# Kernel optimization log

Hardware: AMD Instinct MI355X
Metric: run time of the kernel (lower is better)

## Reference

```python
import jax, jax.numpy as jnp
import numpy as np

B, S, D, H = 2, 4096, 768, 12
DEPTH = D // H


def setup_inputs() -> dict:
    key = jax.random.key(0)
    ks = jax.random.split(key, 6)
    return {
        "q": jax.random.normal(ks[0], (B, S, D), dtype=jnp.float32),
        "k": jax.random.normal(ks[1], (B, S, D), dtype=jnp.float32),
        "v": jax.random.normal(ks[2], (B, S, D), dtype=jnp.float32),
        "wq": jax.random.normal(ks[3], (D, D), dtype=jnp.float32),
        "wk": jax.random.normal(ks[4], (D, D), dtype=jnp.float32),
        "wv": jax.random.normal(ks[5], (D, D), dtype=jnp.float32),
    }


def _split_heads(x):
    # [B, S, D] -> [B, H, S, depth]
    b, s, _ = x.shape
    return x.reshape(b, s, H, DEPTH).transpose(0, 2, 1, 3)


def reference(q, k, v, wq, wk, wv):
    qh = _split_heads(q @ wq)  # [B,H,S,dh]
    kh = _split_heads(k @ wk)
    vh = _split_heads(v @ wv)
    scale = 1.0 / jnp.sqrt(jnp.asarray(DEPTH, dtype=qh.dtype))
    scores = jnp.einsum("bhqd,bhkd->bhqk", qh, kh) * scale  # [B,H,S,S]
    attn = jax.nn.softmax(scores, axis=-1)
    out = jnp.einsum("bhqk,bhkd->bhqd", attn, vh)  # [B,H,S,dh]
    return out.transpose(0, 2, 1, 3).reshape(q.shape[0], -1, D)
```

## Files before the change

### kernel.cpp

```cpp
#include <hip/hip_runtime.h>
#include <cstdint>

#define B_   2
#define S_   4096
#define D_   768
#define H_   12
#define DH_  64
#define BH_  (B_*H_)
#define M_   (B_*S_)

typedef _Float16 fp16;
typedef __attribute__((ext_vector_type(8))) _Float16 fp16x8;
typedef __attribute__((ext_vector_type(4))) _Float16 fp16x4;
typedef __attribute__((ext_vector_type(4))) float    f32x4;

#define MFMA16(a,b,c) __builtin_amdgcn_mfma_f32_16x16x32_f16((a),(b),(c),0,0,0)

__device__ __forceinline__ float exp2_hw(float x) {
  float r; asm("v_exp_f32 %0, %1" : "=v"(r) : "v"(x)); return r;
}
__device__ __forceinline__ uint32_t pkrtz(float a, float b) {
  uint32_t r; asm("v_cvt_pkrtz_f16_f32 %0, %1, %2" : "=v"(r) : "v"(a), "v"(b));
  return r;
}

__device__ __forceinline__ void gld_lds16(const void* g, void* l) {
  __builtin_amdgcn_global_load_lds(
      (const __attribute__((address_space(1))) unsigned int*)g,
      (__attribute__((address_space(3))) unsigned int*)l, 16, 0, 0);
}

__device__ __forceinline__ void stage64x128(const char* gbase, int pitch,
                                            char* lds, int tid) {
  const int lane = tid & 63, wv = tid >> 6;
#pragma unroll
  for (int j = 0; j < 2; ++j) {
    const int o   = (wv*2 + j)*1024 + lane*16;
    const int row = o >> 7;
    const int cb  = (o & 127) ^ ((row & 7) << 4);
    gld_lds16(gbase + (size_t)row*pitch + cb, lds + (wv*2 + j)*1024);
  }
}

__global__ __launch_bounds__(256) void prep_w(const float* __restrict__ wq,
                                              const float* __restrict__ wk,
                                              const float* __restrict__ wv,
                                              fp16* __restrict__ wt) {
  const int idx = blockIdx.x*256 + threadIdx.x;
  const int mat = idx / (768*768);
  const int e   = idx % (768*768);
  const int n   = e / 768, k = e % 768;
  const float* w = mat == 0 ? wq : (mat == 1 ? wk : wv);
  const float v = w[(size_t)k*768 + n];
  fp16* base = wt + (size_t)mat * (2*768*768);
  const fp16 hv = (fp16)v;
  base[e]            = hv;
  base[768*768 + e]  = (fp16)(v - (float)hv);
}

__global__ __launch_bounds__(256) void proj_gemm(
    const float* __restrict__ xq, const float* __restrict__ xk,
    const float* __restrict__ xv, const fp16* __restrict__ wt,
    fp16* __restrict__ qhi, fp16* __restrict__ qlo,
    fp16* __restrict__ khi, fp16* __restrict__ klo,
    fp16* __restrict__ vtp) {
  __shared__ __align__(16) char sm[16384];
  char* sWh = sm;
  char* sWl = sm + 8192;
  const int tid = threadIdx.x, lane = tid & 63, wv = tid >> 6;
  const int c = lane & 15, g = lane >> 4;
  const int r128 = c * 128;
  const int co0 = ((c & 7) ^ g) << 4;
  const int co1 = co0 ^ 64;
  const int mb  = blockIdx.x * 64;
  const int h   = blockIdx.y;
  const int nb  = h * 64;
  const int mat = blockIdx.z;
  const float* x = mat == 0 ? xq : (mat == 1 ? xk : xv);
  const fp16* wth = wt + (size_t)mat * (2*768*768);
  const fp16* wtl = wth + 768*768;

  f32x4 acc[4] = {};
  const int xrow = mb + wv*16 + c;

  for (int k0 = 0; k0 < 768; k0 += 64) {
    __syncthreads();
    stage64x128((const char*)(wth + (size_t)nb*768 + k0), 1536, sWh, tid);
    stage64x128((const char*)(wtl + (size_t)nb*768 + k0), 1536, sWl, tid);
    __syncthreads();

    fp16x8 ah[2], al[2];
#pragma unroll
    for (int ks = 0; ks < 2; ++ks) {
      const float* xp = x + (size_t)xrow*768 + k0 + ks*32 + g*8;
      const f32x4 x0 = *(const f32x4*)xp;
      const f32x4 x1 = *(const f32x4*)(xp + 4);
#pragma unroll
      for (int j = 0; j < 8; ++j) {
        const float v = j < 4 ? x0[j] : x1[j - 4];
        const fp16 hv = (fp16)v;
        ah[ks][j] = hv;
        al[ks][j] = (fp16)(v - (float)hv);
      }
    }
#pragma unroll
    for (int ks = 0; ks < 2; ++ks)
#pragma unroll
      for (int nt = 0; nt < 4; ++nt) {
        const char* wb  = sWh + r128 + nt*2048;
        const char* wlb = sWl + r128 + nt*2048;
        const int co = ks ? co1 : co0;
        const fp16x8 bh = *(const fp16x8*)(wb  + co);
        const fp16x8 bl = *(const fp16x8*)(wlb + co);
        acc[nt] = MFMA16(ah[ks], bh, acc[nt]);
        acc[nt] = MFMA16(ah[ks], bl, acc[nt]);
        acc[nt] = MFMA16(al[ks], bh, acc[nt]);
      }
  }

  if (mat < 2) {
    fp16* ph = mat ? khi : qhi;
    fp16* pl = mat ? klo : qlo;
#pragma unroll
    for (int nt = 0; nt < 4; ++nt)
#pragma unroll
      for (int r = 0; r < 4; ++r) {
        const int m = mb + wv*16 + g*4 + r;
        const int bb = m >> 12, s = m & (S_-1);
        const size_t idx = ((size_t)(bb*H_ + h)*S_ + s)*DH_ + nt*16 + c;
        const float v = acc[nt][r];
        const fp16 hv = (fp16)v;
        ph[idx] = hv;
        pl[idx] = (fp16)(v - (float)hv);
      }
  } else {
    __syncthreads();
    fp16* tile = (fp16*)sm;
#pragma unroll
    for (int nt = 0; nt < 4; ++nt) {
      const int dd = nt*16 + c, ml = wv*16 + g*4;
      const fp16x4 hv = {(fp16)acc[nt][0], (fp16)acc[nt][1],
                         (fp16)acc[nt][2], (fp16)acc[nt][3]};
      *(fp16x4*)(tile + dd*64 + ml) = hv;
    }
    __syncthreads();
    const int bb = mb >> 12, s0 = mb & (S_-1);
    const int dd = tid >> 2, ml0 = (tid & 3) * 16;
    const size_t obase = ((size_t)(bb*H_ + h)*DH_ + dd)*S_ + s0 + ml0;
#pragma unroll
    for (int u = 0; u < 2; ++u)
      *(fp16x8*)(vtp + obase + u*8) = *(const fp16x8*)(tile + dd*64 + ml0 + u*8);
  }
}

__global__ __launch_bounds__(256) void mha_flash(
    const fp16* __restrict__ qhi, const fp16* __restrict__ qlo,
    const fp16* __restrict__ khi, const fp16* __restrict__ klo,
    const fp16* __restrict__ vt, float* __restrict__ out) {
  __shared__ __align__(16) char sm[40960];
  char* sKh = sm;
  char* sKl = sm + 8192;
  char* sV  = sm + 16384;
  char* sP  = sm + 24576;

  const int tid = threadIdx.x, lane = tid & 63, wv = tid >> 6;
  const int c = lane & 15, g = lane >> 4;
  const int r128 = c * 128;
  const int co0 = ((c & 7) ^ g) << 4;
  const int co1 = co0 ^ 64;
  const int pg3 = (g & 1) << 3;
  const int pse = ((c & 7) ^ (g >> 1)) << 4;
  const int qb = blockIdx.x * 128;
  const int bh = blockIdx.y;
  const int b = bh / H_, h = bh % H_;

  const size_t qoff = ((size_t)bh*S_ + qb) * DH_;
  stage64x128((const char*)(qhi + qoff),          128, sm,         tid);
  stage64x128((const char*)(qhi + qoff + 64*DH_), 128, sm +  8192, tid);
  stage64x128((const char*)(qlo + qoff),          128, sm + 16384, tid);
  stage64x128((const char*)(qlo + qoff + 64*DH_), 128, sm + 24576, tid);
  __syncthreads();

  fp16x8 qfh[2][2], qfl[2][2];
  {
    const char* hb = sm + (wv >> 1)*8192;
    const char* lb = sm + 16384 + (wv >> 1)*8192;
#pragma unroll
    for (int qs = 0; qs < 2; ++qs) {
      const int rl = ((wv & 1)*32 + qs*16 + c) * 128;
      qfh[qs][0] = *(const fp16x8*)(hb + rl + co0);
      qfh[qs][1] = *(const fp16x8*)(hb + rl + co1);
      qfl[qs][0] = *(const fp16x8*)(lb + rl + co0);
      qfl[qs][1] = *(const fp16x8*)(lb + rl + co1);
    }
  }

  float m_run[2] = {-1e30f, -1e30f};
  float lrow[2][4] = {};
  f32x4 accO[2][4] = {};
  fp16x8 ones;
#pragma unroll
  for (int j = 0; j < 8; ++j) ones[j] = (fp16)1.0f;
  const float C2 = 0.125f * 1.4426950408889634f;

  for (int kt = 0; kt < S_/64; ++kt) {
    __syncthreads();
    const size_t koff = ((size_t)bh*S_ + kt*64) * DH_;
    stage64x128((const char*)(khi + koff), 128, sKh, tid);
    stage64x128((const char*)(klo + koff), 128, sKl, tid);
    stage64x128((const char*)(vt + (size_t)bh*DH_*S_ + kt*64), S_*2, sV, tid);
    __syncthreads();

    f32x4 accS[2][4] = {};
#pragma unroll
    for (int t = 0; t < 4; ++t) {
      const char* kb = sKh + r128 + t*2048;
      const char* lb = sKl + r128 + t*2048;
      const fp16x8 kh0 = *(const fp16x8*)(kb + co0);
      const fp16x8 kh1 = *(const fp16x8*)(kb + co1);
      const fp16x8 kl0 = *(const fp16x8*)(lb + co0);
      const fp16x8 kl1 = *(const fp16x8*)(lb + co1);
#pragma unroll
      for (int qs = 0; qs < 2; ++qs) {
        accS[qs][t] = MFMA16(kh0, qfh[qs][0], accS[qs][t]);
        accS[qs][t] = MFMA16(kh0, qfl[qs][0], accS[qs][t]);
        accS[qs][t] = MFMA16(kl0, qfh[qs][0], accS[qs][t]);
        accS[qs][t] = MFMA16(kh1, qfh[qs][1], accS[qs][t]);
        accS[qs][t] = MFMA16(kh1, qfl[qs][1], accS[qs][t]);
        accS[qs][t] = MFMA16(kl1, qfh[qs][1], accS[qs][t]);
      }
    }

    float mx0 = -1e30f, mx1 = -1e30f;
#pragma unroll
    for (int t = 0; t < 4; ++t) {
      mx0 = fmaxf(mx0, fmaxf(fmaxf(accS[0][t][0], accS[0][t][1]),
                             fmaxf(accS[0][t][2], accS[0][t][3])));
      mx1 = fmaxf(mx1, fmaxf(fmaxf(accS[1][t][0], accS[1][t][1]),
                             fmaxf(accS[1][t][2], accS[1][t][3])));
    }
    mx0 = fmaxf(mx0, __shfl_xor(mx0, 16));
    mx0 = fmaxf(mx0, __shfl_xor(mx0, 32));
    mx1 = fmaxf(mx1, __shfl_xor(mx1, 16));
    mx1 = fmaxf(mx1, __shfl_xor(mx1, 32));

    const bool rec = (mx0 > m_run[0]) || (mx1 > m_run[1]);
    if (__any(rec)) {
#pragma unroll
      for (int qs = 0; qs < 2; ++qs) {
        const float mxq = qs ? mx1 : mx0;
        const float m_new = fmaxf(m_run[qs], mxq);
        const float corr = exp2_hw(__builtin_fmaf(m_run[qs], C2, -m_new*C2));
        m_run[qs] = m_new;
        float crow[4];
#pragma unroll
        for (int r = 0; r < 4; ++r)
          crow[r] = __shfl(corr, (lane & 48) | (g*4 + r));
#pragma unroll
        for (int r = 0; r < 4; ++r) lrow[qs][r] *= crow[r];
#pragma unroll
        for (int d = 0; d < 4; ++d)
#pragma unroll
          for (int r = 0; r < 4; ++r) accO[qs][d][r] *= crow[r];
      }
    }

    char* pbase = sP + wv*4096 + r128;
#pragma unroll
    for (int qs = 0; qs < 2; ++qs) {
      const float negnm = -m_run[qs]*C2;
      char* pb = pbase + qs*2048;
#pragma unroll
      for (int t = 0; t < 4; ++t) {
        const float p0 = exp2_hw(__builtin_fmaf(accS[qs][t][0], C2, negnm));
        const float p1 = exp2_hw(__builtin_fmaf(accS[qs][t][1], C2, negnm));
        const float p2 = exp2_hw(__builtin_fmaf(accS[qs][t][2], C2, negnm));
        const float p3 = exp2_hw(__builtin_fmaf(accS[qs][t][3], C2, negnm));
        uint2 pw; pw.x = pkrtz(p0, p1); pw.y = pkrtz(p2, p3);
        *(uint2*)(pb + (pg3 | (pse ^ (t*32)))) = pw;
      }
    }

    const fp16x8 pA0 = *(const fp16x8*)(pbase + co0);
    const fp16x8 pA1 = *(const fp16x8*)(pbase + co1);
    const fp16x8 pB0 = *(const fp16x8*)(pbase + 2048 + co0);
    const fp16x8 pB1 = *(const fp16x8*)(pbase + 2048 + co1);
    f32x4 aL0 = {}, aL1 = {};
    aL0 = MFMA16(pA0, ones, aL0);
    aL0 = MFMA16(pA1, ones, aL0);
    aL1 = MFMA16(pB0, ones, aL1);
    aL1 = MFMA16(pB1, ones, aL1);
#pragma unroll
    for (int d = 0; d < 4; ++d) {
      const char* vb = sV + r128 + d*2048;
      const fp16x8 v0 = *(const fp16x8*)(vb + co0);
      const fp16x8 v1 = *(const fp16x8*)(vb + co1);
      accO[0][d] = MFMA16(pA0, v0, accO[0][d]);
      accO[0][d] = MFMA16(pA1, v1, accO[0][d]);
      accO[1][d] = MFMA16(pB0, v0, accO[1][d]);
      accO[1][d] = MFMA16(pB1, v1, accO[1][d]);
    }
#pragma unroll
    for (int r = 0; r < 4; ++r) {
      lrow[0][r] += aL0[r];
      lrow[1][r] += aL1[r];
    }
  }

#pragma unroll
  for (int qs = 0; qs < 2; ++qs) {
    float inv[4];
#pragma unroll
    for (int r = 0; r < 4; ++r) inv[r] = 1.f / lrow[qs][r];
    const int s0 = qb + wv*32 + qs*16 + g*4;
#pragma unroll
    for (int d = 0; d < 4; ++d)
#pragma unroll
      for (int r = 0; r < 4; ++r)
        out[((size_t)(b*S_ + s0 + r))*D_ + h*DH_ + d*16 + c] =
            accO[qs][d][r] * inv[r];
  }
}

extern "C" void kernel_launch(void* const* d_in, const int* in_sizes, int n_in,
                              void* d_out, int out_size, void* d_ws, size_t ws_size,
                              hipStream_t stream) {
  const float* xq = (const float*)d_in[0];
  const float* xk = (const float*)d_in[1];
  const float* xv = (const float*)d_in[2];
  const float* wq = (const float*)d_in[3];
  const float* wk = (const float*)d_in[4];
  const float* wv = (const float*)d_in[5];
  float* out = (float*)d_out;

  fp16* wt  = (fp16*)d_ws;
  fp16* qhi = wt + (size_t)6*768*768;
  const size_t PL = (size_t)BH_*S_*DH_;
  fp16* qlo = qhi + PL;
  fp16* khi = qlo + PL;
  fp16* klo = khi + PL;
  fp16* vtp = klo + PL;

  hipLaunchKernelGGL(prep_w, dim3(3*768*768/256), dim3(256), 0, stream,
                     wq, wk, wv, wt);
  hipLaunchKernelGGL(proj_gemm, dim3(M_/64, H_, 3), dim3(256), 0, stream,
                     xq, xk, xv, wt, qhi, qlo, khi, klo, vtp);
  hipLaunchKernelGGL(mha_flash, dim3(S_/128, BH_), dim3(256), 0, stream,
                     qhi, qlo, khi, klo, vtp, out);
}
```

Before: 514.5 us.

## Double-buffer K tiles, prefetch next K during PV, split P per half

The K hi/lo tiles are now double-buffered. The next tile's K is staged after the mid-iteration barrier, so its global-load latency overlaps the P·V MFMAs. V is staged at the top of each iteration, which removes one of the two leading barriers. The P scratch is halved by processing the two 16-row query halves one after another through the same buffer. s_setprio hints are placed around the MFMA blocks. LDS grows from 40KB to 48KB per block, which may reduce resident blocks per CU.

```diff
diff --git a/kernel.cpp b/kernel.cpp
--- a/kernel.cpp
+++ b/kernel.cpp
@@ -157,11 +157,13 @@
     const fp16* __restrict__ qhi, const fp16* __restrict__ qlo,
     const fp16* __restrict__ khi, const fp16* __restrict__ klo,
     const fp16* __restrict__ vt, float* __restrict__ out) {
-  __shared__ __align__(16) char sm[40960];
-  char* sKh = sm;
-  char* sKl = sm + 8192;
-  char* sV  = sm + 16384;
-  char* sP  = sm + 24576;
+  __shared__ __align__(16) char sm[49152];
+  char* sKh0 = sm;
+  char* sKl0 = sm + 8192;
+  char* sKh1 = sm + 16384;
+  char* sKl1 = sm + 24576;
+  char* sV   = sm + 32768;
+  char* sP   = sm + 40960;
 
   const int tid = threadIdx.x, lane = tid & 63, wv = tid >> 6;
   const int c = lane & 15, g = lane >> 4;
@@ -194,6 +196,13 @@
       qfl[qs][1] = *(const fp16x8*)(lb + rl + co1);
     }
   }
+  __syncthreads();
+
+  const size_t kbase = (size_t)bh * S_ * DH_;
+  const size_t vbase = (size_t)bh * DH_ * S_;
+  stage64x128((const char*)(khi + kbase), 128, sKh0, tid);
+  stage64x128((const char*)(klo + kbase), 128, sKl0, tid);
+  __syncthreads();
 
   float m_run[2] = {-1e30f, -1e30f};
   float lrow[2][4] = {};
@@ -204,18 +213,19 @@
   const float C2 = 0.125f * 1.4426950408889634f;
 
   for (int kt = 0; kt < S_/64; ++kt) {
-    __syncthreads();
-    const size_t koff = ((size_t)bh*S_ + kt*64) * DH_;
-    stage64x128((const char*)(khi + koff), 128, sKh, tid);
-    stage64x128((const char*)(klo + koff), 128, sKl, tid);
-    stage64x128((const char*)(vt + (size_t)bh*DH_*S_ + kt*64), S_*2, sV, tid);
-    __syncthreads();
+    char* sKhC = (kt & 1) ? sKh1 : sKh0;
+    char* sKlC = (kt & 1) ? sKl1 : sKl0;
+    char* sKhN = (kt & 1) ? sKh0 : sKh1;
+    char* sKlN = (kt & 1) ? sKl0 : sKl1;
+
+    stage64x128((const char*)(vt + vbase + kt*64), S_*2, sV, tid);
 
     f32x4 accS[2][4] = {};
+    __builtin_amdgcn_s_setprio(1);
 #pragma unroll
     for (int t = 0; t < 4; ++t) {
-      const char* kb = sKh + r128 + t*2048;
-      const char* lb = sKl + r128 + t*2048;
+      const char* kb = sKhC + r128 + t*2048;
+      const char* lb = sKlC + r128 + t*2048;
       const fp16x8 kh0 = *(const fp16x8*)(kb + co0);
       const fp16x8 kh1 = *(const fp16x8*)(kb + co1);
       const fp16x8 kl0 = *(const fp16x8*)(lb + co0);
@@ -230,6 +240,7 @@
         accS[qs][t] = MFMA16(kl1, qfh[qs][1], accS[qs][t]);
       }
     }
+    __builtin_amdgcn_s_setprio(0);
 
     float mx0 = -1e30f, mx1 = -1e30f;
 #pragma unroll
@@ -265,46 +276,76 @@
       }
     }
 
-    char* pbase = sP + wv*4096 + r128;
-#pragma unroll
-    for (int qs = 0; qs < 2; ++qs) {
-      const float negnm = -m_run[qs]*C2;
-      char* pb = pbase + qs*2048;
+    char* pbase = sP + wv*2048 + r128;
+    {
+      const float negnm = -m_run[0]*C2;
 #pragma unroll
       for (int t = 0; t < 4; ++t) {
-        const float p0 = exp2_hw(__builtin_fmaf(accS[qs][t][0], C2, negnm));
-        const float p1 = exp2_hw(__builtin_fmaf(accS[qs][t][1], C2, negnm));
-        const float p2 = exp2_hw(__builtin_fmaf(accS[qs][t][2], C2, negnm));
-        const float p3 = exp2_hw(__builtin_fmaf(accS[qs][t][3], C2, negnm));
+        const float p0 = exp2_hw(__builtin_fmaf(accS[0][t][0], C2, negnm));
+        const float p1 = exp2_hw(__builtin_fmaf(accS[0][t][1], C2, negnm));
+        const float p2 = exp2_hw(__builtin_fmaf(accS[0][t][2], C2, negnm));
+        const float p3 = exp2_hw(__builtin_fmaf(accS[0][t][3], C2, negnm));
         uint2 pw; pw.x = pkrtz(p0, p1); pw.y = pkrtz(p2, p3);
-        *(uint2*)(pb + (pg3 | (pse ^ (t*32)))) = pw;
-      }
-    }
-
-    const fp16x8 pA0 = *(const fp16x8*)(pbase + co0);
-    const fp16x8 pA1 = *(const fp16x8*)(pbase + co1);
-    const fp16x8 pB0 = *(const fp16x8*)(pbase + 2048 + co0);
-    const fp16x8 pB1 = *(const fp16x8*)(pbase + 2048 + co1);
-    f32x4 aL0 = {}, aL1 = {};
-    aL0 = MFMA16(pA0, ones, aL0);
-    aL0 = MFMA16(pA1, ones, aL0);
-    aL1 = MFMA16(pB0, ones, aL1);
-    aL1 = MFMA16(pB1, ones, aL1);
-#pragma unroll
-    for (int d = 0; d < 4; ++d) {
-      const char* vb = sV + r128 + d*2048;
-      const fp16x8 v0 = *(const fp16x8*)(vb + co0);
-      const fp16x8 v1 = *(const fp16x8*)(vb + co1);
-      accO[0][d] = MFMA16(pA0, v0, accO[0][d]);
-      accO[0][d] = MFMA16(pA1, v1, accO[0][d]);
-      accO[1][d] = MFMA16(pB0, v0, accO[1][d]);
-      accO[1][d] = MFMA16(pB1, v1, accO[1][d]);
-    }
-#pragma unroll
-    for (int r = 0; r < 4; ++r) {
-      lrow[0][r] += aL0[r];
-      lrow[1][r] += aL1[r];
-    }
+        *(uint2*)(pbase + (pg3 | (pse ^ (t*32)))) = pw;
+      }
+    }
+
+    __syncthreads();
+
+    if (kt < S_/64 - 1) {
+      stage64x128((const char*)(khi + kbase + (size_t)(kt+1)*64*DH_), 128,
+                  sKhN, tid);
+      stage64x128((const char*)(klo + kbase + (size_t)(kt+1)*64*DH_), 128,
+                  sKlN, tid);
+    }
+
+    {
+      const fp16x8 pA0 = *(const fp16x8*)(pbase + co0);
+      const fp16x8 pA1 = *(const fp16x8*)(pbase + co1);
+      f32x4 aL = {};
+      aL = MFMA16(pA0, ones, aL);
+      aL = MFMA16(pA1, ones, aL);
+      __builtin_amdgcn_s_setprio(1);
+#pragma unroll
+      for (int d = 0; d < 4; ++d) {
+        const char* vb = sV + r128 + d*2048;
+        accO[0][d] = MFMA16(pA0, *(const fp16x8*)(vb + co0), accO[0][d]);
+        accO[0][d] = MFMA16(pA1, *(const fp16x8*)(vb + co1), accO[0][d]);
+      }
+      __builtin_amdgcn_s_setprio(0);
+#pragma unroll
+      for (int r = 0; r < 4; ++r) lrow[0][r] += aL[r];
+    }
+
+    {
+      const float negnm = -m_run[1]*C2;
+#pragma unroll
+      for (int t = 0; t < 4; ++t) {
+        const float p0 = exp2_hw(__builtin_fmaf(accS[1][t][0], C2, negnm));
+        const float p1 = exp2_hw(__builtin_fmaf(accS[1][t][1], C2, negnm));
+        const float p2 = exp2_hw(__builtin_fmaf(accS[1][t][2], C2, negnm));
+        const float p3 = exp2_hw(__builtin_fmaf(accS[1][t][3], C2, negnm));
+        uint2 pw; pw.x = pkrtz(p0, p1); pw.y = pkrtz(p2, p3);
+        *(uint2*)(pbase + (pg3 | (pse ^ (t*32)))) = pw;
+      }
+      const fp16x8 pB0 = *(const fp16x8*)(pbase + co0);
+      const fp16x8 pB1 = *(const fp16x8*)(pbase + co1);
+      f32x4 aL = {};
+      aL = MFMA16(pB0, ones, aL);
+      aL = MFMA16(pB1, ones, aL);
+      __builtin_amdgcn_s_setprio(1);
+#pragma unroll
+      for (int d = 0; d < 4; ++d) {
+        const char* vb = sV + r128 + d*2048;
+        accO[1][d] = MFMA16(pB0, *(const fp16x8*)(vb + co0), accO[1][d]);
+        accO[1][d] = MFMA16(pB1, *(const fp16x8*)(vb + co1), accO[1][d]);
+      }
+      __builtin_amdgcn_s_setprio(0);
+#pragma unroll
+      for (int r = 0; r < 4; ++r) lrow[1][r] += aL[r];
+    }
+
+    __syncthreads();
   }
 
 #pragma unroll
```

After: 518.7 us. Within noise of the previous version (+0.8%).

## Pre-split activations into fp16 hi/lo planes before projection GEMM

Applied to the files above, without the earlier changes.

Adds a prep kernel that converts q/k/v activations once into fp16 hi and lo planes in workspace. A new projection GEMM stages those planes into LDS with async loads instead of converting fp32 inside each tile. Each activation row is read by 12 head blocks, so the intent is to remove that repeated fp32 load and split work. The cost is an extra pass over the activations plus larger workspace, with a fallback to the old path when the workspace is too small.

```diff
diff --git a/kernel.cpp b/kernel.cpp
--- a/kernel.cpp
+++ b/kernel.cpp
@@ -56,6 +56,120 @@
   const fp16 hv = (fp16)v;
   base[e]            = hv;
   base[768*768 + e]  = (fp16)(v - (float)hv);
+}
+
+__global__ __launch_bounds__(256) void prep_x3(const float* __restrict__ xq,
+                                               const float* __restrict__ xk,
+                                               const float* __restrict__ xv,
+                                               fp16* __restrict__ xh,
+                                               fp16* __restrict__ xl) {
+  const size_t i = ((size_t)blockIdx.x*256 + threadIdx.x) * 8;
+  const size_t MD = (size_t)M_ * D_;
+  const int mat = (int)(i / MD);
+  const size_t e = i - (size_t)mat * MD;
+  const float* x = mat == 0 ? xq : (mat == 1 ? xk : xv);
+  const f32x4 a = *(const f32x4*)(x + e);
+  const f32x4 b = *(const f32x4*)(x + e + 4);
+  fp16x8 hv, lv;
+#pragma unroll
+  for (int j = 0; j < 8; ++j) {
+    const float v = j < 4 ? a[j] : b[j - 4];
+    const fp16 h = (fp16)v;
+    hv[j] = h; lv[j] = (fp16)(v - (float)h);
+  }
+  *(fp16x8*)(xh + i) = hv;
+  *(fp16x8*)(xl + i) = lv;
+}
+
+__global__ __launch_bounds__(256) void proj_gemmA3(
+    const fp16* __restrict__ xh3, const fp16* __restrict__ xl3,
+    const fp16* __restrict__ wt,
+    fp16* __restrict__ qhi, fp16* __restrict__ qlo,
+    fp16* __restrict__ khi, fp16* __restrict__ klo,
+    fp16* __restrict__ vtp) {
+  __shared__ __align__(16) char sm[32768];
+  char* sXh = sm;
+  char* sXl = sm + 8192;
+  char* sWh = sm + 16384;
+  char* sWl = sm + 24576;
+  const int tid = threadIdx.x, lane = tid & 63, wv = tid >> 6;
+  const int c = lane & 15, g = lane >> 4;
+  const int r128 = c * 128;
+  const int co0 = ((c & 7) ^ g) << 4;
+  const int co1 = co0 ^ 64;
+  const int mb  = blockIdx.x * 64;
+  const int h   = blockIdx.y;
+  const int nb  = h * 64;
+  const int mat = blockIdx.z;
+  const fp16* xh = xh3 + (size_t)mat * M_ * D_;
+  const fp16* xl = xl3 + (size_t)mat * M_ * D_;
+  const fp16* wth = wt + (size_t)mat * (2*768*768);
+  const fp16* wtl = wth + 768*768;
+
+  f32x4 acc[4] = {};
+  for (int k0 = 0; k0 < 768; k0 += 64) {
+    __syncthreads();
+    stage64x128((const char*)(xh  + (size_t)mb*768 + k0), 1536, sXh, tid);
+    stage64x128((const char*)(xl  + (size_t)mb*768 + k0), 1536, sXl, tid);
+    stage64x128((const char*)(wth + (size_t)nb*768 + k0), 1536, sWh, tid);
+    stage64x128((const char*)(wtl + (size_t)nb*768 + k0), 1536, sWl, tid);
+    __syncthreads();
+
+    const int arow = (wv*16 + c) * 128;
+    const fp16x8 ah0 = *(const fp16x8*)(sXh + arow + co0);
+    const fp16x8 ah1 = *(const fp16x8*)(sXh + arow + co1);
+    const fp16x8 al0 = *(const fp16x8*)(sXl + arow + co0);
+    const fp16x8 al1 = *(const fp16x8*)(sXl + arow + co1);
+#pragma unroll
+    for (int nt = 0; nt < 4; ++nt) {
+      const char* wb  = sWh + r128 + nt*2048;
+      const char* wlb = sWl + r128 + nt*2048;
+      const fp16x8 bh0 = *(const fp16x8*)(wb  + co0);
+      const fp16x8 bh1 = *(const fp16x8*)(wb  + co1);
+      const fp16x8 bl0 = *(const fp16x8*)(wlb + co0);
+      const fp16x8 bl1 = *(const fp16x8*)(wlb + co1);
+      acc[nt] = MFMA16(ah0, bh0, acc[nt]);
+      acc[nt] = MFMA16(ah0, bl0, acc[nt]);
+      acc[nt] = MFMA16(al0, bh0, acc[nt]);
+      acc[nt] = MFMA16(ah1, bh1, acc[nt]);
+      acc[nt] = MFMA16(ah1, bl1, acc[nt]);
+      acc[nt] = MFMA16(al1, bh1, acc[nt]);
+    }
+  }
+
+  if (mat < 2) {
+    fp16* ph = mat ? khi : qhi;
+    fp16* pl = mat ? klo : qlo;
+#pragma unroll
+    for (int nt = 0; nt < 4; ++nt)
+#pragma unroll
+      for (int r = 0; r < 4; ++r) {
+        const int m = mb + wv*16 + g*4 + r;
+        const int bb = m >> 12, s = m & (S_-1);
+        const size_t idx = ((size_t)(bb*H_ + h)*S_ + s)*DH_ + nt*16 + c;
+        const float v = acc[nt][r];
+        const fp16 hv = (fp16)v;
+        ph[idx] = hv;
+        pl[idx] = (fp16)(v - (float)hv);
+      }
+  } else {
+    __syncthreads();
+    fp16* tile = (fp16*)sm;
+#pragma unroll
+    for (int nt = 0; nt < 4; ++nt) {
+      const int dd = nt*16 + c, ml = wv*16 + g*4;
+      const fp16x4 hv = {(fp16)acc[nt][0], (fp16)acc[nt][1],
+                         (fp16)acc[nt][2], (fp16)acc[nt][3]};
+      *(fp16x4*)(tile + dd*64 + ml) = hv;
+    }
+    __syncthreads();
+    const int bb = mb >> 12, s0 = mb & (S_-1);
+    const int dd = tid >> 2, ml0 = (tid & 3) * 16;
+    const size_t obase = ((size_t)(bb*H_ + h)*DH_ + dd)*S_ + s0 + ml0;
+#pragma unroll
+    for (int u = 0; u < 2; ++u)
+      *(fp16x8*)(vtp + obase + u*8) = *(const fp16x8*)(tile + dd*64 + ml0 + u*8);
+  }
 }
 
 __global__ __launch_bounds__(256) void proj_gemm(
@@ -340,11 +454,24 @@
   fp16* khi = qlo + PL;
   fp16* klo = khi + PL;
   fp16* vtp = klo + PL;
+  fp16* xh3 = vtp + PL;
+  const size_t XP = (size_t)3 * M_ * D_;
+  fp16* xl3 = xh3 + XP;
+  const size_t need = (size_t)((char*)(xl3 + XP) - (char*)d_ws);
 
   hipLaunchKernelGGL(prep_w, dim3(3*768*768/256), dim3(256), 0, stream,
                      wq, wk, wv, wt);
-  hipLaunchKernelGGL(proj_gemm, dim3(M_/64, H_, 3), dim3(256), 0, stream,
-                     xq, xk, xv, wt, qhi, qlo, khi, klo, vtp);
+
+  if (ws_size >= need) {
+    hipLaunchKernelGGL(prep_x3, dim3((int)(XP/(256*8))), dim3(256), 0, stream,
+                       xq, xk, xv, xh3, xl3);
+    hipLaunchKernelGGL(proj_gemmA3, dim3(M_/64, H_, 3), dim3(256), 0, stream,
+                       xh3, xl3, wt, qhi, qlo, khi, klo, vtp);
+  } else {
+    hipLaunchKernelGGL(proj_gemm, dim3(M_/64, H_, 3), dim3(256), 0, stream,
+                       xq, xk, xv, wt, qhi, qlo, khi, klo, vtp);
+  }
+
   hipLaunchKernelGGL(mha_flash, dim3(S_/128, BH_), dim3(256), 0, stream,
                      qhi, qlo, khi, klo, vtp, out);
 }
```

After: 538.1 us. 1.05x slower.
